# Kernel optimization log

Measured on AMD Instinct MI355X. Metric: run time of the kernel, lower is better.

The kernel has to match this reference:

```python
import jax, jax.numpy as jnp
import numpy as np
from math import sqrt

B, S, E, H = 2, 2048, 768, 12
DH = E // H
W = 256            # one-sided attention window (attention_window=512)
G = 16             # number of global tokens (positions 0..G-1 in every batch row)
PAD = 128          # last PAD tokens per row are padding (masked)
FF = 3072          # SwiGLU intermediate size
NEG = -1e9
EPS = 1e-5


def _ln(x, g, b):
    m = jnp.mean(x, axis=-1, keepdims=True)
    v = jnp.var(x, axis=-1, keepdims=True)
    return (x - m) * jax.lax.rsqrt(v + EPS) * g + b


def _rope(x, t):
    # x: [B,H,S,DH]; t: [B,S] float 'set positions'
    half = DH // 2
    inv_freq = 1.0 / (10000.0 ** (jnp.arange(half, dtype=jnp.float32) / half))
    ang = t[:, None, :, None] * inv_freq            # [B,1,S,half]
    cos, sin = jnp.cos(ang), jnp.sin(ang)
    x1, x2 = x[..., :half], x[..., half:]
    return jnp.concatenate([x1 * cos - x2 * sin, x2 * cos + x1 * sin], axis=-1)


def _heads(x):  # [B,S,E] -> [B,H,S,DH]
    return x.reshape(B, S, H, DH).transpose(0, 2, 1, 3)


def _chunk3(x):
    # [B,H,S,D] -> [B,H,C,3W,D]: for query chunk c, keys from chunks c-1,c,c+1 (zero padded)
    b, h, s, d = x.shape
    c = s // W
    xp = jnp.pad(x, ((0, 0), (0, 0), (W, W), (0, 0))).reshape(b, h, c + 2, W, d)
    return jnp.concatenate([xp[:, :, :-2], xp[:, :, 1:-1], xp[:, :, 2:]], axis=3)


def _forward(x, attention_mask, global_attention_mask,
             Wq, bq, Wk, bk, Wv, bv, Wqg, bqg, Wkg, bkg, Wvg, bvg,
             ln0_g, ln0_b, ln1_g, ln1_b, W1, W3, W2):
    C = S // W
    merged = attention_mask * (global_attention_mask + 1)   # 0 masked, 1 local, 2 global
    is_masked = merged == 0
    is_global = merged == 2
    remove = merged != 1   # keys removed from windowed attention (masked or global)

    q = _heads(x @ Wq + bq) / sqrt(DH)
    k = _heads(x @ Wk + bk)
    v = _heads(x @ Wv + bv)

    # RoPE over 'set positions': (~is_index_masked) * cumsum(is_index_global_attn)
    t = jnp.where(is_masked, 0, jnp.cumsum(is_global.astype(jnp.int32), axis=1)).astype(jnp.float32)
    q = _rope(q, t)
    k = _rope(k, t)

    # --- sliding-window (banded) scores: band[b,h,i,d] = q_i . k_{i+d-W} ---
    qc = q.reshape(B, H, C, W, DH)
    k3 = _chunk3(k)
    s3 = jnp.einsum('bhcpd,bhcqd->bhcpq', qc, k3)                     # [B,H,C,W,3W]
    didx = jnp.arange(W)[:, None] + jnp.arange(2 * W + 1)[None, :]    # [W,2W+1]
    band = jnp.take_along_axis(s3, didx[None, None, None], axis=-1)   # [B,H,C,W,2W+1]

    # mask removed keys / out-of-range positions inside the band
    rmp = jnp.pad(remove, ((0, 0), (W, W)), constant_values=True).reshape(B, C + 2, W)
    rm3 = jnp.concatenate([rmp[:, :-2], rmp[:, 1:-1], rmp[:, 2:]], axis=2)  # [B,C,3W]
    band_rm = jnp.take_along_axis(jnp.broadcast_to(rm3[:, :, None, :], (B, C, W, 3 * W)),
                                  didx[None, None], axis=-1)                # [B,C,W,2W+1]
    band = jnp.where(band_rm[:, None], NEG, band).reshape(B, H, S, 2 * W + 1)

    # --- global-key columns (keys taken from the RoPE'd local key vectors) ---
    sg = jnp.einsum('bhid,bhgd->bhig', q, k[:, :, :G])                # [B,H,S,G]

    scores = jnp.concatenate([sg, band], axis=-1)                     # [B,H,S,G+2W+1]
    probs = jax.nn.softmax(scores.astype(jnp.float32), axis=-1).astype(x.dtype)
    probs = jnp.where(is_masked[:, None, :, None], 0.0, probs)

    # --- probs @ value: global columns + band ---
    out = jnp.einsum('bhig,bhgd->bhid', probs[..., :G], v[:, :, :G])
    pl = probs[..., G:].reshape(B, H, C, W, 2 * W + 1)
    rows = jnp.broadcast_to(jnp.arange(W)[:, None], (W, 2 * W + 1))
    p3 = jnp.zeros((B, H, C, W, 3 * W), probs.dtype).at[:, :, :, rows, didx].set(pl)
    v3 = _chunk3(v)
    out = out + jnp.einsum('bhcpq,bhcqd->bhcpd', p3, v3).reshape(B, H, S, DH)
    attn = out.transpose(0, 2, 1, 3).reshape(B, S, E)

    # --- full attention for global tokens (separate global projections, no RoPE) ---
    gq = _heads(x @ Wqg + bqg)[:, :, :G] / sqrt(DH)                   # [B,H,G,DH]
    gk = _heads(x @ Wkg + bkg)
    gv = _heads(x @ Wvg + bvg)
    gs = jnp.einsum('bhgd,bhjd->bhgj', gq, gk)                        # [B,H,G,S]
    gs = jnp.where(is_masked[:, None, None, :], NEG, gs)
    gp = jax.nn.softmax(gs.astype(jnp.float32), axis=-1).astype(x.dtype)
    gout = jnp.einsum('bhgj,bhjd->bhgd', gp, gv).transpose(0, 2, 1, 3).reshape(B, G, E)
    attn = attn.at[:, :G].set(gout)

    # residual + post-LN, SwiGLU FFN, residual + post-LN (dropout = eval mode)
    h0 = _ln(x + attn, ln0_g, ln0_b)
    ffn = (jax.nn.silu(h0 @ W1) * (h0 @ W3)) @ W2
    return _ln(h0 + ffn, ln1_g, ln1_b)


def setup_inputs():
    key = jax.random.key(0)
    ks = jax.random.split(key, 12)
    x = jax.random.normal(ks[0], (B, S, E), jnp.float32)
    attention_mask = jnp.ones((B, S), jnp.int32).at[:, S - PAD:].set(0)
    global_attention_mask = jnp.zeros((B, S), jnp.int32).at[:, :G].set(1)
    sd = 0.02
    def w(k, shape):
        return jax.random.normal(k, shape, jnp.float32) * sd
    return dict(
        x=x, attention_mask=attention_mask, global_attention_mask=global_attention_mask,
        Wq=w(ks[1], (E, E)), bq=jnp.zeros((E,), jnp.float32),
        Wk=w(ks[2], (E, E)), bk=jnp.zeros((E,), jnp.float32),
        Wv=w(ks[3], (E, E)), bv=jnp.zeros((E,), jnp.float32),
        Wqg=w(ks[4], (E, E)), bqg=jnp.zeros((E,), jnp.float32),
        Wkg=w(ks[5], (E, E)), bkg=jnp.zeros((E,), jnp.float32),
        Wvg=w(ks[6], (E, E)), bvg=jnp.zeros((E,), jnp.float32),
        ln0_g=jnp.ones((E,), jnp.float32), ln0_b=jnp.zeros((E,), jnp.float32),
        ln1_g=jnp.ones((E,), jnp.float32), ln1_b=jnp.zeros((E,), jnp.float32),
        W1=w(ks[7], (E, FF)), W3=w(ks[8], (E, FF)), W2=w(ks[9], (FF, E)))


def reference(x, attention_mask, global_attention_mask, Wq, bq, Wk, bk, Wv, bv,
              Wqg, bqg, Wkg, bkg, Wvg, bvg, ln0_g, ln0_b, ln1_g, ln1_b, W1, W3, W2):
    return _forward(x, attention_mask, global_attention_mask,
                    Wq, bq, Wk, bk, Wv, bv, Wqg, bqg, Wkg, bkg, Wvg, bvg,
                    ln0_g, ln0_b, ln1_g, ln1_b, W1, W3, W2)
```

## Files before the change

kernel.cpp:

```cpp
#include <hip/hip_runtime.h>


#define BB_ 2
#define SS 2048
#define EE 768
#define HH 12
#define DHH 64
#define GG 16
#define FFN 3072
#define MM (BB_*SS)

typedef __bf16 bf16_t;
typedef __bf16 bf16x8_t __attribute__((ext_vector_type(8)));
typedef float f32x4_t __attribute__((ext_vector_type(4)));

__device__ inline void gload16(const void* g, void* l) {
  __builtin_amdgcn_global_load_lds((const __attribute__((address_space(1))) void*)g,
                                   (__attribute__((address_space(3))) void*)l, 16, 0, 0);
}

__global__ __launch_bounds__(64) void detect_kernel(const unsigned int* __restrict__ w,
                                                    int* __restrict__ flag) {
  int cnt = 0;
  for (int i = threadIdx.x; i < 1024; i += 64) {
    unsigned e = (w[i] >> 7) & 0xFF;
    cnt += (e >= 100 && e <= 144) ? 1 : 0;
  }
  for (int off = 32; off; off >>= 1) cnt += __shfl_xor(cnt, off);
  if (threadIdx.x == 0) flag[0] = (cnt > 512) ? 1 : 0;
}

struct CanonP { const void* src[11]; bf16_t* dst[11]; };

__global__ __launch_bounds__(256) void canon_kernel(CanonP P, const int* __restrict__ flag) {
  constexpr int ns[11] = {3145728, 768,768,768,768,768,768, 768,768,768,768};
  int idx4 = (blockIdx.x*256 + threadIdx.x)*4;
  const bool isb = flag[0] != 0;
  int off = 0, seg = -1, loc = 0;
  #pragma unroll
  for (int i=0;i<11;i++) {
    if (seg < 0 && idx4 < off + ns[i]) { seg = i; loc = idx4 - off; }
    off += ns[i];
  }
  if (seg < 0) return;
  const void* s = P.src[seg];
  bf16_t* d = P.dst[seg];
  if (isb) {
    *(uint2*)&d[loc] = *(const uint2*)((const unsigned short*)s + loc);
  } else {
    float4 v = *(const float4*)((const float*)s + loc);
    d[loc+0] = (bf16_t)v.x; d[loc+1] = (bf16_t)v.y;
    d[loc+2] = (bf16_t)v.z; d[loc+3] = (bf16_t)v.w;
  }
}

struct TP6 { const void* s[6]; bf16_t* d[6]; };

__global__ __launch_bounds__(256) void trans_kernel(TP6 P, int R, int C,
                                                    const int* __restrict__ flag) {
  const int z = blockIdx.z;
  const void* src = P.s[z]; bf16_t* dst = P.d[z];
  const bool isb = flag[0] != 0;
  __shared__ bf16_t tile[32][33];
  int tx = threadIdx.x & 31, ty = threadIdx.x >> 5;
  int r0 = blockIdx.y*32, c0 = blockIdx.x*32;
  #pragma unroll
  for (int i=0;i<4;i++) {
    int rr = ty + i*8;
    size_t si = (size_t)(r0+rr)*C + c0 + tx;
    tile[rr][tx] = isb ? ((const bf16_t*)src)[si] : (bf16_t)((const float*)src)[si];
  }
  __syncthreads();
  #pragma unroll
  for (int i=0;i<4;i++) {
    int cc = ty + i*8;
    dst[(size_t)(c0+cc)*R + r0 + tx] = tile[tx][cc];
  }
}

__global__ __launch_bounds__(256) void zero_kernel(float* __restrict__ p, int n) {
  int i = blockIdx.x*256 + threadIdx.x;
  if (i < n) p[i] = 0.f;
}

__global__ __launch_bounds__(256) void flags_kernel(const int* __restrict__ am,
                                                    const int* __restrict__ gm,
                                                    float* __restrict__ tpos,
                                                    int* __restrict__ flags) {
  int b = blockIdx.x;
  int t = threadIdx.x;
  int lane = t & 63, wv = t >> 6;
  int base = b*SS + t*8;
  int mg[8]; int isg[8]; int loc = 0;
  for (int i=0;i<8;i++) {
    int a = am[base+i], g = gm[base+i];
    int merged = a*(g+1);
    mg[i] = merged;
    isg[i] = (merged==2) ? 1 : 0;
    loc += isg[i];
  }
  int x = loc;
  for (int off=1; off<64; off<<=1) {
    int y = __shfl_up(x, off);
    if (lane >= off) x += y;
  }
  __shared__ int wtot[4];
  if (lane==63) wtot[wv] = x;
  __syncthreads();
  int prev = 0;
  for (int w=0; w<wv; w++) prev += wtot[w];
  int run = prev + x - loc;
  for (int i=0;i<8;i++) {
    run += isg[i];
    int masked = (mg[i]==0) ? 1 : 0;
    int glob   = (mg[i]==2) ? 1 : 0;
    int rem    = (mg[i]!=1) ? 1 : 0;
    tpos[base+i]  = masked ? 0.f : (float)run;
    flags[base+i] = masked | (glob<<1) | (rem<<2);
  }
}

__device__ inline void gemm128_core(const bf16_t* __restrict__ A,
                                    const bf16_t* __restrict__ BT,
                                    int ldA, int ldB, int kbeg, int kend,
                                    int m0, int n0,
                                    bf16_t* As, bf16_t* Bs,
                                    f32x4_t (&acc)[4][4]) {
  const int t = threadIdx.x;
  const int lane = t & 63, wv = t >> 6;
  const int l15 = lane & 15, quad = lane >> 4;
  const int wr = (wv >> 1) << 6, wc = (wv & 1) << 6;
  const int rsub = lane >> 3, pch = lane & 7;
  const int sch = pch ^ rsub;
  const size_t abase = (size_t)(m0 + wv*32 + rsub)*ldA + sch*8;
  const size_t bbase = (size_t)(n0 + wv*32 + rsub)*ldB + sch*8;
  const int sx = l15 & 7;
  bf16_t* lA = As + (wv*32)*64;
  bf16_t* lB = Bs + (wv*32)*64;
  for (int k0 = kbeg; k0 < kend; k0 += 64) {
    __syncthreads();
    #pragma unroll
    for (int j=0;j<4;j++) {
      gload16(A + abase + (size_t)(j*8)*ldA + k0, lA + j*8*64);
      gload16(BT + bbase + (size_t)(j*8)*ldB + k0, lB + j*8*64);
    }
    __syncthreads();
    #pragma unroll
    for (int c=0;c<2;c++) {
      bf16x8_t af[4], bfr[4];
      #pragma unroll
      for (int a=0;a<4;a++)
        af[a] = *(const bf16x8_t*)&As[(wr + a*16 + l15)*64 + ((c*4+quad)^sx)*8];
      #pragma unroll
      for (int b=0;b<4;b++)
        bfr[b] = *(const bf16x8_t*)&Bs[(wc + b*16 + l15)*64 + ((c*4+quad)^sx)*8];
      #pragma unroll
      for (int a=0;a<4;a++)
        #pragma unroll
        for (int b=0;b<4;b++)
          acc[a][b] = __builtin_amdgcn_mfma_f32_16x16x32_bf16(af[a], bfr[b], acc[a][b], 0,0,0);
    }
  }
}

struct ProjParams {
  const bf16_t* W[5];
  const bf16_t* Bi[5];
  bf16_t* O[5];
};

__global__ __launch_bounds__(256) void proj_kernel(const bf16_t* __restrict__ x,
                                                   ProjParams P,
                                                   const float* __restrict__ tpos) {
  const int m0 = blockIdx.x*128, n0 = blockIdx.y*128;
  const int z  = blockIdx.z;
  __shared__ bf16_t As[128*64];
  __shared__ bf16_t Bs[128*64];
  f32x4_t acc[4][4];
  #pragma unroll
  for (int a=0;a<4;a++)
    #pragma unroll
    for (int b=0;b<4;b++) acc[a][b] = (f32x4_t){0.f,0.f,0.f,0.f};
  gemm128_core(x, P.W[z], EE, EE, 0, EE, m0, n0, As, Bs, acc);

  const int t = threadIdx.x;
  const int lane = t & 63, wv = t >> 6;
  const int l15 = lane & 15, quad = lane >> 4;
  const int wr = (wv >> 1) << 6, wc = (wv & 1) << 6;
  const float scale = (z==0) ? 0.125f : 1.f;
  const bool rope = (z<2);
  const int h = (n0 + wc) >> 6;
  bf16_t* Oz = P.O[z];
  const bf16_t* Bz = P.Bi[z];
  float bvals[4];
  #pragma unroll
  for (int b=0;b<4;b++) bvals[b] = (float)Bz[h*64 + b*16 + l15];
  #pragma unroll
  for (int a=0;a<4;a++) {
    #pragma unroll
    for (int r=0;r<4;r++) {
      int row = m0 + wr + a*16 + quad*4 + r;
      int bb = row >> 11, spos = row & (SS-1);
      float vals[4];
      #pragma unroll
      for (int b=0;b<4;b++) vals[b] = (acc[a][b][r] + bvals[b]) * scale;
      if (rope) {
        float tv = tpos[row];
        #pragma unroll
        for (int b=0;b<2;b++) {
          int j = b*16 + l15;
          float inv = __expf(-(float)j * (9.210340371976184f/32.f));
          float ang = tv * inv;
          float sn = __sinf(ang), cs = __cosf(ang);
          float x1 = vals[b], x2 = vals[b+2];
          vals[b]   = x1*cs - x2*sn;
          vals[b+2] = x2*cs + x1*sn;
        }
      }
      bf16_t* dst = Oz + ((size_t)(bb*HH + h)*SS + spos)*DHH;
      #pragma unroll
      for (int b=0;b<4;b++) dst[b*16 + l15] = (bf16_t)vals[b];
    }
  }
}

__global__ __launch_bounds__(256) void gemm_ffn13(const bf16_t* __restrict__ A,
                                                  const bf16_t* __restrict__ B1T,
                                                  const bf16_t* __restrict__ B3T,
                                                  bf16_t* __restrict__ g1) {
  const int n0 = blockIdx.x*64, m0 = blockIdx.y*128;
  __shared__ bf16_t As[128*64];
  __shared__ bf16_t Bs1[64*64];
  __shared__ bf16_t Bs3[64*64];
  const int t = threadIdx.x;
  const int lane = t & 63, wv = t >> 6;
  const int l15 = lane & 15, quad = lane >> 4;
  const int wr = (wv >> 1) << 6, wc = (wv & 1) << 5;
  const int rsub = lane >> 3, pch = lane & 7;
  const int sch = pch ^ rsub;
  const size_t abase = (size_t)(m0 + wv*32 + rsub)*EE + sch*8;
  const size_t bbase = (size_t)(n0 + wv*16 + rsub)*EE + sch*8;
  const int sx = l15 & 7;
  bf16_t* lA  = As  + (wv*32)*64;
  bf16_t* lB1 = Bs1 + (wv*16)*64;
  bf16_t* lB3 = Bs3 + (wv*16)*64;
  f32x4_t a1[4][2], a3[4][2];
  #pragma unroll
  for (int a=0;a<4;a++)
    #pragma unroll
    for (int b=0;b<2;b++) { a1[a][b] = (f32x4_t){0.f,0.f,0.f,0.f};
                            a3[a][b] = (f32x4_t){0.f,0.f,0.f,0.f}; }
  for (int k0 = 0; k0 < EE; k0 += 64) {
    __syncthreads();
    #pragma unroll
    for (int j=0;j<4;j++)
      gload16(A + abase + (size_t)(j*8)*EE + k0, lA + j*8*64);
    #pragma unroll
    for (int j=0;j<2;j++) {
      gload16(B1T + bbase + (size_t)(j*8)*EE + k0, lB1 + j*8*64);
      gload16(B3T + bbase + (size_t)(j*8)*EE + k0, lB3 + j*8*64);
    }
    __syncthreads();
    #pragma unroll
    for (int c=0;c<2;c++) {
      bf16x8_t af[4], b1f[2], b3f[2];
      #pragma unroll
      for (int a=0;a<4;a++)
        af[a] = *(const bf16x8_t*)&As[(wr + a*16 + l15)*64 + ((c*4+quad)^sx)*8];
      #pragma unroll
      for (int b=0;b<2;b++) {
        b1f[b] = *(const bf16x8_t*)&Bs1[(wc + b*16 + l15)*64 + ((c*4+quad)^sx)*8];
        b3f[b] = *(const bf16x8_t*)&Bs3[(wc + b*16 + l15)*64 + ((c*4+quad)^sx)*8];
      }
      #pragma unroll
      for (int a=0;a<4;a++)
        #pragma unroll
        for (int b=0;b<2;b++) {
          a1[a][b] = __builtin_amdgcn_mfma_f32_16x16x32_bf16(af[a], b1f[b], a1[a][b], 0,0,0);
          a3[a][b] = __builtin_amdgcn_mfma_f32_16x16x32_bf16(af[a], b3f[b], a3[a][b], 0,0,0);
        }
    }
  }
  #pragma unroll
  for (int a=0;a<4;a++)
    #pragma unroll
    for (int r=0;r<4;r++) {
      int row = m0 + wr + a*16 + quad*4 + r;
      #pragma unroll
      for (int b=0;b<2;b++) {
        float tv = a1[a][b][r];
        float sil = tv / (1.f + __expf(-tv));
        g1[(size_t)row*FFN + n0 + wc + b*16 + l15] = (bf16_t)(sil * a3[a][b][r]);
      }
    }
}

struct Ffn2Out { float* p[4]; };

__global__ __launch_bounds__(256) void gemm_ffn2(const bf16_t* __restrict__ A,
                                                 const bf16_t* __restrict__ BT,
                                                 Ffn2Out O) {
  const int m0 = blockIdx.x*128, n0 = blockIdx.y*128;
  const int kz = blockIdx.z;
  __shared__ bf16_t As[128*64];
  __shared__ bf16_t Bs[128*64];
  f32x4_t acc[4][4];
  #pragma unroll
  for (int a=0;a<4;a++)
    #pragma unroll
    for (int b=0;b<4;b++) acc[a][b] = (f32x4_t){0.f,0.f,0.f,0.f};
  gemm128_core(A, BT, FFN, FFN, kz*768, (kz+1)*768, m0, n0, As, Bs, acc);
  const int t = threadIdx.x;
  const int lane = t & 63, wv = t >> 6;
  const int l15 = lane & 15, quad = lane >> 4;
  const int wr = (wv >> 1) << 6, wc = (wv & 1) << 6;
  float* C = O.p[kz];
  #pragma unroll
  for (int a=0;a<4;a++)
    #pragma unroll
    for (int r=0;r<4;r++) {
      int row = m0 + wr + a*16 + quad*4 + r;
      #pragma unroll
      for (int b=0;b<4;b++)
        C[(size_t)row*EE + n0 + wc + b*16 + l15] = acc[a][b][r];
    }
}

__global__ __launch_bounds__(64) void qg_kernel(const bf16_t* __restrict__ x,
                                                const bf16_t* __restrict__ WqgT,
                                                const bf16_t* __restrict__ bqg,
                                                float* __restrict__ qgb) {
  int g = blockIdx.x, h = blockIdx.y, b = blockIdx.z;
  int d = threadIdx.x;
  __shared__ float xs[EE];
  for (int i=d; i<EE; i+=64) xs[i] = (float)x[((size_t)b*SS + g)*EE + i];
  __syncthreads();
  float acc = 0.f;
  const bf16_t* wrow = WqgT + (size_t)(h*64+d)*EE;
  #pragma unroll 4
  for (int k=0;k<EE;k+=8) {
    bf16x8_t w8 = *(const bf16x8_t*)(wrow + k);
    #pragma unroll
    for (int i=0;i<8;i++) acc += xs[k+i] * (float)w8[i];
  }
  acc = (acc + (float)bqg[h*64+d]) * 0.125f;
  qgb[((size_t)(b*HH+h)*GG + g)*DHH + d] = acc;
}

__global__ __launch_bounds__(256) void band_kernel(const bf16_t* __restrict__ qb,
                                                   const bf16_t* __restrict__ kb,
                                                   const bf16_t* __restrict__ vb,
                                                   const int* __restrict__ flags,
                                                   float* __restrict__ attn) {
  const int flat = blockIdx.x;
  const int nb = (flat & 7) * 96 + (flat >> 3);
  const int px = nb & 31;
  const int hb = nb >> 5;
  const int h = hb % HH, b = hb / HH;
  const int p0 = px * 64;

  const int t = threadIdx.x;
  const int wv = t>>6, lane = t&63;
  const int l15 = lane & 15, quad = lane >> 4;
  const size_t bh = (size_t)(b*HH+h);
  const bf16_t* kbh = kb + bh*SS*DHH;
  const bf16_t* vbh = vb + bh*SS*DHH;
  const int* fl = flags + b*SS;
  const int q0 = p0 + wv*16;

  __shared__ bf16_t Ks[2][64*DHH];
  __shared__ bf16_t Vt[2][64*72];
  __shared__ bf16_t Pw[4][16*72];

  const bf16_t* qrow = qb + (bh*SS + q0 + l15)*DHH;
  bf16x8_t qa0 = *(const bf16x8_t*)(qrow + quad*8);
  bf16x8_t qa1 = *(const bf16x8_t*)(qrow + 32 + quad*8);

  const int srsub = lane >> 3, spch = lane & 7;
  const int vkp  = (t & 31) * 2;
  const int vdh0 = (t >> 5) * 8;

  {
    const int kb0 = p0 - 256;
    #pragma unroll
    for (int j=0;j<2;j++) {
      int row = wv*16 + j*8 + srsub;
      int kc = min(max(kb0 + row, 0), SS-1);
      gload16(kbh + (size_t)kc*DHH + (spch ^ srsub)*8, &Ks[0][(wv*16 + j*8)*DHH]);
    }
    int kc1 = min(max(kb0 + vkp,   0), SS-1);
    int kc2 = min(max(kb0 + vkp+1, 0), SS-1);
    bf16x8_t v1 = *(const bf16x8_t*)(vbh + (size_t)kc1*DHH + vdh0);
    bf16x8_t v2 = *(const bf16x8_t*)(vbh + (size_t)kc2*DHH + vdh0);
    #pragma unroll
    for (int i=0;i<8;i++) {
      union { unsigned u; bf16_t hh[2]; } pk;
      pk.hh[0] = v1[i]; pk.hh[1] = v2[i];
      *(unsigned*)&Vt[0][(vdh0+i)*72 + vkp] = pk.u;
    }
  }
  __syncthreads();

  f32x4_t o[4];
  #pragma unroll
  for (int i=0;i<4;i++) o[i] = (f32x4_t){0.f,0.f,0.f,0.f};
  float lsum[4] = {0.f,0.f,0.f,0.f};
  bf16_t* P = Pw[wv];

  for (int unit=0; unit<10; unit++) {
    const int cur = unit & 1, nxt = cur ^ 1;
    const int kb0 = (unit<9) ? (p0 - 256 + unit*64) : 0;
    const bool pre = (unit < 9);
    bf16x8_t pv1, pv2;
    if (pre) {
      const int kbn = (unit < 8) ? (kb0 + 64) : 0;
      #pragma unroll
      for (int j=0;j<2;j++) {
        int row = wv*16 + j*8 + srsub;
        int kc = min(max(kbn + row, 0), SS-1);
        gload16(kbh + (size_t)kc*DHH + (spch ^ srsub)*8, &Ks[nxt][(wv*16 + j*8)*DHH]);
      }
      int kc1 = min(max(kbn + vkp,   0), SS-1);
      int kc2 = min(max(kbn + vkp+1, 0), SS-1);
      pv1 = *(const bf16x8_t*)(vbh + (size_t)kc1*DHH + vdh0);
      pv2 = *(const bf16x8_t*)(vbh + (size_t)kc2*DHH + vdh0);
    }
    const bf16_t* Kc = Ks[cur];
    const int nsub = (unit<9) ? 4 : 1;
    for (int sub=0; sub<4; sub++) {
      if (sub < nsub) {
        int krow = sub*16 + l15;
        int kpos = kb0 + krow;
        bf16x8_t kf0 = *(const bf16x8_t*)&Kc[krow*DHH + (((quad  ) ^ (krow&7))<<3)];
        bf16x8_t kf1 = *(const bf16x8_t*)&Kc[krow*DHH + (((quad+4) ^ (krow&7))<<3)];
        f32x4_t s = (f32x4_t){0.f,0.f,0.f,0.f};
        s = __builtin_amdgcn_mfma_f32_16x16x32_bf16(qa0, kf0, s, 0,0,0);
        s = __builtin_amdgcn_mfma_f32_16x16x32_bf16(qa1, kf1, s, 0,0,0);
        int kc = min(max(kpos,0),SS-1);
        bool drop = false;
        if (unit<9) drop = (kpos<0) || (kpos>=SS) || (((fl[kc]>>2)&1)!=0);
        #pragma unroll
        for (int r=0;r<4;r++) {
          float e;
          if (unit==9) {
            e = __expf(s[r]);
          } else {
            int dj = kpos - (q0 + quad*4 + r);
            bool valid = (dj>=-256) && (dj<=256) && (!drop);
            e = valid ? __expf(s[r]) : 0.f;
          }
          lsum[r] += e;
          P[(quad*4+r)*72 + sub*16 + l15] = (bf16_t)e;
        }
      } else {
        #pragma unroll
        for (int r=0;r<4;r++) P[(quad*4+r)*72 + sub*16 + l15] = (bf16_t)0.f;
      }
    }
    __builtin_amdgcn_s_setprio(1);
    #pragma unroll
    for (int chunk=0; chunk<2; chunk++) {
      bf16x8_t pf = *(const bf16x8_t*)&P[l15*72 + chunk*32 + quad*8];
      #pragma unroll
      for (int nt=0; nt<4; nt++) {
        bf16x8_t vf = *(const bf16x8_t*)&Vt[cur][(nt*16+l15)*72 + chunk*32 + quad*8];
        o[nt] = __builtin_amdgcn_mfma_f32_16x16x32_bf16(pf, vf, o[nt], 0,0,0);
      }
    }
    __builtin_amdgcn_s_setprio(0);
    if (pre) {
      #pragma unroll
      for (int i=0;i<8;i++) {
        union { unsigned u; bf16_t hh[2]; } pk;
        pk.hh[0] = pv1[i]; pk.hh[1] = pv2[i];
        *(unsigned*)&Vt[nxt][(vdh0+i)*72 + vkp] = pk.u;
      }
      __syncthreads();
    }
  }
  #pragma unroll
  for (int r=0;r<4;r++) {
    float s = lsum[r];
    s += __shfl_xor(s,1); s += __shfl_xor(s,2);
    s += __shfl_xor(s,4); s += __shfl_xor(s,8);
    lsum[r] = s;
  }
  #pragma unroll
  for (int r=0;r<4;r++) {
    int q = q0 + quad*4 + r;
    int masked = fl[q] & 1;
    float inv = masked ? 0.f : 1.f/lsum[r];
    float* dst = attn + ((size_t)(b*SS+q))*EE + h*64 + l15;
    #pragma unroll
    for (int nt=0; nt<4; nt++) dst[nt*16] = o[nt][r]*inv;
  }
}

__global__ __launch_bounds__(256) void gattn_part(const float* __restrict__ qgb,
                                                  const bf16_t* __restrict__ kgb,
                                                  const bf16_t* __restrict__ vgb,
                                                  const int* __restrict__ flags,
                                                  float* __restrict__ go,
                                                  float* __restrict__ gl) {
  const int kbase = blockIdx.x*128;
  const int h = blockIdx.y, b = blockIdx.z;
  const int t = threadIdx.x;
  __shared__ float gqs[16*68];
  __shared__ float Ks[64*68];
  __shared__ float Vs[64*68];
  __shared__ float es[16*64];
  const size_t bh = (size_t)(b*HH+h);
  #pragma unroll
  for (int j=0;j<4;j++) {
    int idx = t + j*256;
    int g = idx>>6, d = idx&63;
    gqs[g*68+d] = qgb[(bh*GG + g)*DHH + d];
  }
  float accv[4] = {0.f,0.f,0.f,0.f};
  float lpart = 0.f;
  const int gs = t>>4, kslot = t&15;
  const int dp = t&63, grp = t>>6;
  const bf16_t* kb_ = kgb + bh*SS*DHH;
  const bf16_t* vb_ = vgb + bh*SS*DHH;
  const int* fl = flags + b*SS;
  for (int tile=0; tile<2; tile++) {
    int k0 = kbase + tile*64;
    __syncthreads();
    {
      int row = t>>2, seg = t&3;
      const bf16_t* sk = kb_ + (size_t)(k0+row)*DHH + seg*16;
      const bf16_t* sv = vb_ + (size_t)(k0+row)*DHH + seg*16;
      bf16x8_t k1 = *(const bf16x8_t*)sk;
      bf16x8_t k2 = *(const bf16x8_t*)(sk+8);
      bf16x8_t v1 = *(const bf16x8_t*)sv;
      bf16x8_t v2 = *(const bf16x8_t*)(sv+8);
      #pragma unroll
      for (int i=0;i<8;i++) {
        Ks[row*68 + seg*16 + i]     = (float)k1[i];
        Ks[row*68 + seg*16 + 8 + i] = (float)k2[i];
        Vs[row*68 + seg*16 + i]     = (float)v1[i];
        Vs[row*68 + seg*16 + 8 + i] = (float)v2[i];
      }
    }
    __syncthreads();
    #pragma unroll
    for (int j=0;j<4;j++) {
      int key = kslot + 16*j;
      const float* gq = &gqs[gs*68];
      const float* kr = &Ks[key*68];
      float s = 0.f;
      #pragma unroll
      for (int d4=0; d4<64; d4+=4) {
        float4 a = *(const float4*)(gq + d4);
        float4 kk = *(const float4*)(kr + d4);
        s += a.x*kk.x + a.y*kk.y + a.z*kk.z + a.w*kk.w;
      }
      int msk = fl[k0+key] & 1;
      float e = msk ? 0.f : __expf(s);
      es[gs*64+key] = e;
      lpart += e;
    }
    __syncthreads();
    #pragma unroll
    for (int g=0; g<4; g++) {
      int gg = grp*4+g;
      float a = accv[g];
      for (int key=0;key<64;key++) a += es[gg*64+key]*Vs[key*68+dp];
      accv[g] = a;
    }
  }
  __syncthreads();
  es[gs*64 + kslot] = lpart;
  __syncthreads();
  if (t < 16) {
    float s = 0.f;
    for (int j=0;j<16;j++) s += es[t*64+j];
    atomicAdd(&gl[bh*16 + t], s);
  }
  #pragma unroll
  for (int g=0; g<4; g++)
    atomicAdd(&go[(bh*16 + grp*4+g)*64 + dp], accv[g]);
}

__global__ __launch_bounds__(256) void addln_kernel(const bf16_t* __restrict__ Abf,
                                                    const float* __restrict__ Af,
                                                    const float* __restrict__ B0,
                                                    const float* __restrict__ B1,
                                                    const float* __restrict__ B2,
                                                    const float* __restrict__ B3,
                                                    const float* __restrict__ gof,
                                                    const float* __restrict__ glf,
                                                    const bf16_t* __restrict__ gw,
                                                    const bf16_t* __restrict__ bw,
                                                    float* __restrict__ outf,
                                                    bf16_t* __restrict__ outb,
                                                    const int* __restrict__ flagp) {
  int r = blockIdx.x, t = threadIdx.x;
  int lane = t&63, wv = t>>6;
  int spos = r & (SS-1), bb = r >> 11;
  bool isglob = (gof != nullptr) && (spos < GG);
  float v[3]; float sum=0.f, ss=0.f;
  #pragma unroll
  for (int j=0;j<3;j++) {
    int idx = t + j*256;
    size_t gi = (size_t)r*EE+idx;
    float a = Abf ? (float)Abf[gi] : Af[gi];
    float bv;
    if (isglob) {
      int hh = idx >> 6, dp = idx & 63;
      int slot = (bb*HH + hh)*GG + spos;
      bv = gof[(size_t)slot*DHH + dp] / glf[slot];
    } else {
      bv = B0[gi];
    }
    float val = a + bv;
    if (B1) val += B1[gi];
    if (B2) val += B2[gi];
    if (B3) val += B3[gi];
    v[j] = val; sum += val; ss += val*val;
  }
  #pragma unroll
  for (int off=32; off>=1; off>>=1) {
    sum += __shfl_xor(sum, off);
    ss  += __shfl_xor(ss, off);
  }
  __shared__ float s1[4], s2[4];
  if (lane==0) { s1[wv]=sum; s2[wv]=ss; }
  __syncthreads();
  sum = s1[0]+s1[1]+s1[2]+s1[3];
  ss  = s2[0]+s2[1]+s2[2]+s2[3];
  float mean = sum * (1.f/(float)EE);
  float var  = ss * (1.f/(float)EE) - mean*mean;
  float rstd = rsqrtf(var + 1e-5f);
  bool wantb, wantf;
  if (flagp) { bool isb = (*flagp)!=0; wantb = isb; wantf = !isb; }
  else { wantb = (outb!=nullptr); wantf = (outf!=nullptr); }
  #pragma unroll
  for (int j=0;j<3;j++) {
    int idx = t + j*256;
    float o = (v[j]-mean)*rstd*(float)gw[idx] + (float)bw[idx];
    if (wantf) outf[(size_t)r*EE+idx] = o;
    if (wantb) outb[(size_t)r*EE+idx] = (bf16_t)o;
  }
}

extern "C" void kernel_launch(void* const* d_in, const int* in_sizes, int n_in,
                              void* d_out, int out_size, void* d_ws, size_t ws_size,
                              hipStream_t stream) {
  const void* x_r    = d_in[0];
  const int* am      = (const int*)d_in[1];
  const int* gm      = (const int*)d_in[2];
  (void)in_sizes; (void)n_in; (void)out_size; (void)ws_size;

  char* ws = (char*)d_ws;
  size_t off = 0;
  auto alloc = [&](size_t bytes) -> void* {
    void* p = ws + off;
    off += (bytes + 255) & ~(size_t)255;
    return p;
  };
  bf16_t* xc    = (bf16_t*)alloc((size_t)MM*EE*2);
  bf16_t* WT[6]; bf16_t* bc[6];
  for (int i=0;i<6;i++) { WT[i] = (bf16_t*)alloc((size_t)EE*EE*2); bc[i] = (bf16_t*)alloc(EE*2); }
  bf16_t* lnc[4];
  for (int i=0;i<4;i++) lnc[i] = (bf16_t*)alloc(EE*2);
  bf16_t* W1T = (bf16_t*)alloc((size_t)EE*FFN*2);
  bf16_t* W3T = (bf16_t*)alloc((size_t)EE*FFN*2);
  bf16_t* W2T = (bf16_t*)alloc((size_t)FFN*EE*2);
  const size_t NBHSD = (size_t)BB_*HH*SS*DHH;
  bf16_t* qb    = (bf16_t*)alloc(NBHSD*2);
  bf16_t* kb    = (bf16_t*)alloc(NBHSD*2);
  bf16_t* vb    = (bf16_t*)alloc(NBHSD*2);
  bf16_t* kgb   = (bf16_t*)alloc(NBHSD*2);
  bf16_t* vgb   = (bf16_t*)alloc(NBHSD*2);
  float* qgb   = (float*)alloc((size_t)BB_*HH*GG*DHH*4);
  float* attn  = (float*)alloc((size_t)MM*EE*4);
  float* h0f   = (float*)alloc((size_t)MM*EE*4);
  bf16_t* h0b  = (bf16_t*)alloc((size_t)MM*EE*2);
  bf16_t* g1   = (bf16_t*)alloc((size_t)MM*FFN*2);
  float* p3    = (float*)alloc((size_t)MM*EE*4);
  float* go    = (float*)alloc((size_t)BB_*HH*GG*DHH*4);
  float* gl    = (float*)alloc((size_t)BB_*HH*GG*4);
  float* tposb = (float*)alloc((size_t)BB_*SS*4);
  int*   flagb = (int*)alloc((size_t)BB_*SS*4);
  int*   dflag = (int*)alloc(256);
  float* p1 = (float*)qb;
  float* p2 = (float*)qb + (size_t)MM*EE;

  detect_kernel<<<1, 64, 0, stream>>>((const unsigned int*)d_in[3], dflag);

  CanonP CP;
  const void* csrc[11] = { x_r, d_in[4], d_in[6], d_in[8], d_in[10], d_in[12], d_in[14],
                           d_in[15], d_in[16], d_in[17], d_in[18] };
  bf16_t* cdst[11] = { xc, bc[0], bc[1], bc[2], bc[3], bc[4], bc[5],
                       lnc[0], lnc[1], lnc[2], lnc[3] };
  for (int i=0;i<11;i++) { CP.src[i]=csrc[i]; CP.dst[i]=cdst[i]; }
  canon_kernel<<<3081, 256, 0, stream>>>(CP, dflag);

  TP6 T6;
  const int wi[6] = {3,5,7,9,11,13};
  for (int i=0;i<6;i++) { T6.s[i]=d_in[wi[i]]; T6.d[i]=WT[i]; }
  trans_kernel<<<dim3(24,24,6), 256, 0, stream>>>(T6, EE, EE, dflag);
  TP6 TF; TF.s[0]=d_in[19]; TF.d[0]=W1T; TF.s[1]=d_in[20]; TF.d[1]=W3T;
  for (int i=2;i<6;i++) { TF.s[i]=d_in[19]; TF.d[i]=W1T; }
  trans_kernel<<<dim3(96,24,2), 256, 0, stream>>>(TF, EE, FFN, dflag);
  TP6 T2; T2.s[0]=d_in[21]; T2.d[0]=W2T;
  for (int i=1;i<6;i++) { T2.s[i]=d_in[21]; T2.d[i]=W2T; }
  trans_kernel<<<dim3(24,96,1), 256, 0, stream>>>(T2, FFN, EE, dflag);

  zero_kernel<<<98, 256, 0, stream>>>(go, 24960);

  flags_kernel<<<BB_, 256, 0, stream>>>(am, gm, tposb, flagb);

  ProjParams P;
  P.W[0]=WT[0]; P.Bi[0]=bc[0]; P.O[0]=qb;
  P.W[1]=WT[1]; P.Bi[1]=bc[1]; P.O[1]=kb;
  P.W[2]=WT[2]; P.Bi[2]=bc[2]; P.O[2]=vb;
  P.W[3]=WT[4]; P.Bi[3]=bc[4]; P.O[3]=kgb;
  P.W[4]=WT[5]; P.Bi[4]=bc[5]; P.O[4]=vgb;
  proj_kernel<<<dim3(MM/128, EE/128, 5), 256, 0, stream>>>(xc, P, tposb);

  qg_kernel<<<dim3(GG, HH, BB_), 64, 0, stream>>>(xc, WT[3], bc[3], qgb);

  band_kernel<<<dim3(768), 256, 0, stream>>>(qb, kb, vb, flagb, attn);

  gattn_part<<<dim3(SS/128, HH, BB_), 256, 0, stream>>>(qgb, kgb, vgb, flagb, go, gl);

  addln_kernel<<<MM, 256, 0, stream>>>(xc, nullptr, attn, nullptr, nullptr, nullptr,
                                       go, gl, lnc[0], lnc[1], h0f, h0b, nullptr);

  gemm_ffn13<<<dim3(FFN/64, MM/128), 256, 0, stream>>>(h0b, W1T, W3T, g1);
  Ffn2Out FO; FO.p[0]=attn; FO.p[1]=p1; FO.p[2]=p2; FO.p[3]=p3;
  gemm_ffn2<<<dim3(MM/128, EE/128, 4), 256, 0, stream>>>(g1, W2T, FO);

  addln_kernel<<<MM, 256, 0, stream>>>(nullptr, h0f, attn, p1, p2, p3,
                                       nullptr, nullptr, lnc[2], lnc[3],
                                       (float*)d_out, (bf16_t*)d_out, dflag);
}
```

Before: 353.1 us.

## Double band-attention query tile per block and fold zeroing into flags kernel

The band attention kernel now handles 128 queries per block (32 per wave, as two 16-row groups), so each staged K/V tile is reused by twice as many queries. The window now spans 10 key tiles instead of 9 for twice the queries, which cuts K/V load traffic per query. The cost is more registers, a larger P buffer in shared memory, and half as many blocks (384) to spread across CUs. Separately, the zero-fill kernel is merged into the flags kernel as extra blocks, saving one launch.

```diff
diff --git a/kernel.cpp b/kernel.cpp
--- a/kernel.cpp
+++ b/kernel.cpp
@@ -78,16 +78,19 @@
   }
 }
 
-__global__ __launch_bounds__(256) void zero_kernel(float* __restrict__ p, int n) {
-  int i = blockIdx.x*256 + threadIdx.x;
-  if (i < n) p[i] = 0.f;
-}
-
 __global__ __launch_bounds__(256) void flags_kernel(const int* __restrict__ am,
                                                     const int* __restrict__ gm,
                                                     float* __restrict__ tpos,
-                                                    int* __restrict__ flags) {
-  int b = blockIdx.x;
+                                                    int* __restrict__ flags,
+                                                    float* __restrict__ zbuf,
+                                                    int zn) {
+  int blk = blockIdx.x;
+  if (blk >= BB_) {
+    int i = (blk - BB_)*256 + threadIdx.x;
+    if (i < zn) zbuf[i] = 0.f;
+    return;
+  }
+  int b = blk;
   int t = threadIdx.x;
   int lane = t & 63, wv = t >> 6;
   int base = b*SS + t*8;
@@ -353,11 +356,11 @@
                                                    const int* __restrict__ flags,
                                                    float* __restrict__ attn) {
   const int flat = blockIdx.x;
-  const int nb = (flat & 7) * 96 + (flat >> 3);
-  const int px = nb & 31;
-  const int hb = nb >> 5;
+  const int nb = (flat & 7) * 48 + (flat >> 3);
+  const int px = nb & 15;
+  const int hb = nb >> 4;
   const int h = hb % HH, b = hb / HH;
-  const int p0 = px * 64;
+  const int p0 = px * 128;
 
   const int t = threadIdx.x;
   const int wv = t>>6, lane = t&63;
@@ -366,15 +369,19 @@
   const bf16_t* kbh = kb + bh*SS*DHH;
   const bf16_t* vbh = vb + bh*SS*DHH;
   const int* fl = flags + b*SS;
-  const int q0 = p0 + wv*16;
+  const int qbase = p0 + wv*32;
 
   __shared__ bf16_t Ks[2][64*DHH];
   __shared__ bf16_t Vt[2][64*72];
-  __shared__ bf16_t Pw[4][16*72];
-
-  const bf16_t* qrow = qb + (bh*SS + q0 + l15)*DHH;
-  bf16x8_t qa0 = *(const bf16x8_t*)(qrow + quad*8);
-  bf16x8_t qa1 = *(const bf16x8_t*)(qrow + 32 + quad*8);
+  __shared__ bf16_t Pw[4][32*72];
+
+  bf16x8_t qa[2][2];
+  #pragma unroll
+  for (int g=0; g<2; g++) {
+    const bf16_t* qrow = qb + (bh*SS + qbase + g*16 + l15)*DHH;
+    qa[g][0] = *(const bf16x8_t*)(qrow + quad*8);
+    qa[g][1] = *(const bf16x8_t*)(qrow + 32 + quad*8);
+  }
 
   const int srsub = lane >> 3, spch = lane & 7;
   const int vkp  = (t & 31) * 2;
@@ -401,19 +408,21 @@
   }
   __syncthreads();
 
-  f32x4_t o[4];
-  #pragma unroll
-  for (int i=0;i<4;i++) o[i] = (f32x4_t){0.f,0.f,0.f,0.f};
-  float lsum[4] = {0.f,0.f,0.f,0.f};
+  f32x4_t o[2][4];
+  #pragma unroll
+  for (int g=0; g<2; g++)
+    #pragma unroll
+    for (int i=0;i<4;i++) o[g][i] = (f32x4_t){0.f,0.f,0.f,0.f};
+  float lsum[2][4] = {{0.f,0.f,0.f,0.f},{0.f,0.f,0.f,0.f}};
   bf16_t* P = Pw[wv];
 
-  for (int unit=0; unit<10; unit++) {
+  for (int unit=0; unit<11; unit++) {
     const int cur = unit & 1, nxt = cur ^ 1;
-    const int kb0 = (unit<9) ? (p0 - 256 + unit*64) : 0;
-    const bool pre = (unit < 9);
+    const int kb0 = (unit<10) ? (p0 - 256 + unit*64) : 0;
+    const bool pre = (unit < 10);
     bf16x8_t pv1, pv2;
     if (pre) {
-      const int kbn = (unit < 8) ? (kb0 + 64) : 0;
+      const int kbn = (unit < 9) ? (kb0 + 64) : 0;
       #pragma unroll
       for (int j=0;j<2;j++) {
         int row = wv*16 + j*8 + srsub;
@@ -426,45 +435,53 @@
       pv2 = *(const bf16x8_t*)(vbh + (size_t)kc2*DHH + vdh0);
     }
     const bf16_t* Kc = Ks[cur];
-    const int nsub = (unit<9) ? 4 : 1;
+    const int nsub = (unit<10) ? 4 : 1;
     for (int sub=0; sub<4; sub++) {
       if (sub < nsub) {
         int krow = sub*16 + l15;
         int kpos = kb0 + krow;
         bf16x8_t kf0 = *(const bf16x8_t*)&Kc[krow*DHH + (((quad  ) ^ (krow&7))<<3)];
         bf16x8_t kf1 = *(const bf16x8_t*)&Kc[krow*DHH + (((quad+4) ^ (krow&7))<<3)];
-        f32x4_t s = (f32x4_t){0.f,0.f,0.f,0.f};
-        s = __builtin_amdgcn_mfma_f32_16x16x32_bf16(qa0, kf0, s, 0,0,0);
-        s = __builtin_amdgcn_mfma_f32_16x16x32_bf16(qa1, kf1, s, 0,0,0);
         int kc = min(max(kpos,0),SS-1);
         bool drop = false;
-        if (unit<9) drop = (kpos<0) || (kpos>=SS) || (((fl[kc]>>2)&1)!=0);
+        if (unit<10) drop = (kpos<0) || (kpos>=SS) || (((fl[kc]>>2)&1)!=0);
         #pragma unroll
-        for (int r=0;r<4;r++) {
-          float e;
-          if (unit==9) {
-            e = __expf(s[r]);
-          } else {
-            int dj = kpos - (q0 + quad*4 + r);
-            bool valid = (dj>=-256) && (dj<=256) && (!drop);
-            e = valid ? __expf(s[r]) : 0.f;
+        for (int g=0; g<2; g++) {
+          f32x4_t s = (f32x4_t){0.f,0.f,0.f,0.f};
+          s = __builtin_amdgcn_mfma_f32_16x16x32_bf16(qa[g][0], kf0, s, 0,0,0);
+          s = __builtin_amdgcn_mfma_f32_16x16x32_bf16(qa[g][1], kf1, s, 0,0,0);
+          #pragma unroll
+          for (int r=0;r<4;r++) {
+            float e;
+            if (unit==10) {
+              e = __expf(s[r]);
+            } else {
+              int dj = kpos - (qbase + g*16 + quad*4 + r);
+              bool valid = (dj>=-256) && (dj<=256) && (!drop);
+              e = valid ? __expf(s[r]) : 0.f;
+            }
+            lsum[g][r] += e;
+            P[(g*16 + quad*4 + r)*72 + sub*16 + l15] = (bf16_t)e;
           }
-          lsum[r] += e;
-          P[(quad*4+r)*72 + sub*16 + l15] = (bf16_t)e;
         }
       } else {
         #pragma unroll
-        for (int r=0;r<4;r++) P[(quad*4+r)*72 + sub*16 + l15] = (bf16_t)0.f;
+        for (int g=0; g<2; g++)
+          #pragma unroll
+          for (int r=0;r<4;r++) P[(g*16 + quad*4 + r)*72 + sub*16 + l15] = (bf16_t)0.f;
       }
     }
     __builtin_amdgcn_s_setprio(1);
     #pragma unroll
-    for (int chunk=0; chunk<2; chunk++) {
-      bf16x8_t pf = *(const bf16x8_t*)&P[l15*72 + chunk*32 + quad*8];
-      #pragma unroll
-      for (int nt=0; nt<4; nt++) {
-        bf16x8_t vf = *(const bf16x8_t*)&Vt[cur][(nt*16+l15)*72 + chunk*32 + quad*8];
-        o[nt] = __builtin_amdgcn_mfma_f32_16x16x32_bf16(pf, vf, o[nt], 0,0,0);
+    for (int g=0; g<2; g++) {
+      #pragma unroll
+      for (int chunk=0; chunk<2; chunk++) {
+        bf16x8_t pf = *(const bf16x8_t*)&P[(g*16 + l15)*72 + chunk*32 + quad*8];
+        #pragma unroll
+        for (int nt=0; nt<4; nt++) {
+          bf16x8_t vf = *(const bf16x8_t*)&Vt[cur][(nt*16+l15)*72 + chunk*32 + quad*8];
+          o[g][nt] = __builtin_amdgcn_mfma_f32_16x16x32_bf16(pf, vf, o[g][nt], 0,0,0);
+        }
       }
     }
     __builtin_amdgcn_s_setprio(0);
@@ -479,20 +496,23 @@
     }
   }
   #pragma unroll
-  for (int r=0;r<4;r++) {
-    float s = lsum[r];
-    s += __shfl_xor(s,1); s += __shfl_xor(s,2);
-    s += __shfl_xor(s,4); s += __shfl_xor(s,8);
-    lsum[r] = s;
-  }
-  #pragma unroll
-  for (int r=0;r<4;r++) {
-    int q = q0 + quad*4 + r;
-    int masked = fl[q] & 1;
-    float inv = masked ? 0.f : 1.f/lsum[r];
-    float* dst = attn + ((size_t)(b*SS+q))*EE + h*64 + l15;
-    #pragma unroll
-    for (int nt=0; nt<4; nt++) dst[nt*16] = o[nt][r]*inv;
+  for (int g=0; g<2; g++) {
+    #pragma unroll
+    for (int r=0;r<4;r++) {
+      float s = lsum[g][r];
+      s += __shfl_xor(s,1); s += __shfl_xor(s,2);
+      s += __shfl_xor(s,4); s += __shfl_xor(s,8);
+      lsum[g][r] = s;
+    }
+    #pragma unroll
+    for (int r=0;r<4;r++) {
+      int q = qbase + g*16 + quad*4 + r;
+      int masked = fl[q] & 1;
+      float inv = masked ? 0.f : 1.f/lsum[g][r];
+      float* dst = attn + ((size_t)(b*SS+q))*EE + h*64 + l15;
+      #pragma unroll
+      for (int nt=0; nt<4; nt++) dst[nt*16] = o[g][nt][r]*inv;
+    }
   }
 }
 
@@ -708,9 +728,7 @@
   for (int i=1;i<6;i++) { T2.s[i]=d_in[21]; T2.d[i]=W2T; }
   trans_kernel<<<dim3(24,96,1), 256, 0, stream>>>(T2, FFN, EE, dflag);
 
-  zero_kernel<<<98, 256, 0, stream>>>(go, 24960);
-
-  flags_kernel<<<BB_, 256, 0, stream>>>(am, gm, tposb, flagb);
+  flags_kernel<<<BB_ + 98, 256, 0, stream>>>(am, gm, tposb, flagb, go, 24960);
 
   ProjParams P;
   P.W[0]=WT[0]; P.Bi[0]=bc[0]; P.O[0]=qb;
@@ -722,7 +740,7 @@
 
   qg_kernel<<<dim3(GG, HH, BB_), 64, 0, stream>>>(xc, WT[3], bc[3], qgb);
 
-  band_kernel<<<dim3(768), 256, 0, stream>>>(qb, kb, vb, flagb, attn);
+  band_kernel<<<dim3(384), 256, 0, stream>>>(qb, kb, vb, flagb, attn);
 
   gattn_part<<<dim3(SS/128, HH, BB_), 256, 0, stream>>>(qgb, kgb, vgb, flagb, go, gl);
 
```

New measurement: 353.2 us. Within noise of the previous version (+0.0%).
